# Kernel tuning notes

Measured on AMD Instinct MI355X. Metric: run time of the kernel, lower is better.

## Reference

```python
import jax, jax.numpy as jnp
import numpy as np

N = 5000      # nodes
E = 80000     # edges (avg degree 16)
B = 8         # batch of graph signals sharing one graph
IN = 30       # input feature dim (10 steps x 3)
H = 4         # attention heads
D = 64        # hidden dim per head
HD = H * D    # 256
OUT = 3       # output features per step
NUM_GAT_LAYERS = 4  # num_layer=5 -> 1 + (5-2) layers
EPS = 1e-5


def setup_inputs() -> dict:
    key = jax.random.key(0)
    ks = jax.random.split(key, 40)
    inp = {}
    inp["xx"] = jax.random.normal(ks[0], (B, N, IN), dtype=jnp.float32)
    inp["src"] = jax.random.randint(ks[1], (E,), 0, N, dtype=jnp.int32)
    inp["dst"] = jax.random.randint(ks[2], (E,), 0, N, dtype=jnp.int32)
    dims = [IN, HD, HD, HD]
    k = 3
    for l in range(NUM_GAT_LAYERS):
        fan_in = dims[l]
        inp[f"W{l}"] = jax.random.normal(ks[k], (fan_in, HD), dtype=jnp.float32) / np.sqrt(fan_in); k += 1
        inp[f"al{l}"] = jax.random.normal(ks[k], (H, D), dtype=jnp.float32) * 0.1; k += 1
        inp[f"ar{l}"] = jax.random.normal(ks[k], (H, D), dtype=jnp.float32) * 0.1; k += 1
        inp[f"gamma{l}"] = jnp.ones((HD,), dtype=jnp.float32)
        inp[f"beta{l}"] = jnp.zeros((HD,), dtype=jnp.float32)
    inp["W_out"] = jax.random.normal(ks[k], (HD, OUT), dtype=jnp.float32) / np.sqrt(HD); k += 1
    inp["b_out"] = jnp.zeros((OUT,), dtype=jnp.float32)
    inp["output_length"] = 5
    return inp


def _gat_conv(x, W, al, ar, src, dst):
    # DGL GATConv: fc -> per-head attn logits -> edge softmax over dst -> scatter-sum
    h = (x @ W).reshape(N, H, D)                       # [N,H,D]
    el = (h * al).sum(-1)                              # [N,H]
    er = (h * ar).sum(-1)                              # [N,H]
    e = jax.nn.leaky_relu(el[src] + er[dst], 0.2)      # [E,H]
    m = jax.ops.segment_max(e, dst, num_segments=N)    # [N,H] (stable softmax)
    ex = jnp.exp(e - m[dst])                           # [E,H]
    s = jax.ops.segment_sum(ex, dst, num_segments=N)   # [N,H]
    alpha = ex / s[dst]                                # [E,H]
    return jax.ops.segment_sum(alpha[:, :, None] * h[src], dst, num_segments=N)  # [N,H,D]


def _gat_layer(x, W, al, ar, gamma, beta, src, dst):
    # per-sample GATConv, flatten heads, BatchNorm1d (training stats) over (B,N), LeakyReLU
    out = jax.vmap(lambda xb: _gat_conv(xb, W, al, ar, src, dst))(x)  # [B,N,H,D]
    out = out.reshape(B, N, HD)
    mu = out.mean(axis=(0, 1))
    var = out.var(axis=(0, 1))  # biased, matches torch BN normalization
    out = (out - mu) * jax.lax.rsqrt(var + EPS) * gamma + beta
    return jax.nn.leaky_relu(out, 0.01)


def reference(xx, src, dst,
              W0, al0, ar0, gamma0, beta0,
              W1, al1, ar1, gamma1, beta1,
              W2, al2, ar2, gamma2, beta2,
              W3, al3, ar3, gamma3, beta3,
              W_out, b_out, output_length):
    layers = [(W0, al0, ar0, gamma0, beta0),
              (W1, al1, ar1, gamma1, beta1),
              (W2, al2, ar2, gamma2, beta2),
              (W3, al3, ar3, gamma3, beta3)]
    outputs = []
    for _ in range(output_length):
        h = xx
        for (W, al, ar, g, b) in layers:
            h = _gat_layer(h, W, al, ar, g, b, src, dst)
        out = h @ W_out + b_out                      # [B,N,OUT]
        xx = jnp.concatenate([xx[:, :, 3:], out], axis=-1)
        outputs.append(out[:, :, None, :])
    return jnp.concatenate(outputs, axis=2)          # [B,N,T,OUT]
```

## Files before the change

### kernel.cpp

```cpp
#include <hip/hip_runtime.h>
#include <math.h>

#define NNODES 5000
#define NEDGES 80000
#define NB 8
#define NIN 30
#define K0PAD 32
#define NH 4
#define ND 64
#define NHD 256
#define NT 5
#define NOUT 3
#define ROWS (NB * NNODES)
#define BNEPS 1e-5f
#define KP 40
#define NREP 64
#define BM 32
#define CSTR 264

#define GLOBAL_AS __attribute__((address_space(1)))
#define LDS_AS __attribute__((address_space(3)))

typedef short shortx8 __attribute__((ext_vector_type(8)));
typedef _Float16 halfx8 __attribute__((ext_vector_type(8)));
typedef _Float16 halfx4 __attribute__((ext_vector_type(4)));
typedef _Float16 halfx2 __attribute__((ext_vector_type(2)));
typedef float floatx4 __attribute__((ext_vector_type(4)));
typedef int intx4 __attribute__((ext_vector_type(4)));

static __device__ __forceinline__ unsigned short f2h(float f) {
    union { _Float16 h; unsigned short u; } v;
    v.h = (_Float16)f;
    return v.u;
}
static __device__ __forceinline__ float h2f(unsigned short u) {
    union { _Float16 h; unsigned short u; } v;
    v.u = u;
    return (float)v.h;
}
static __device__ __forceinline__ halfx8 splat8(_Float16 x) {
    return (halfx8){x, x, x, x, x, x, x, x};
}


__global__ void count_kernel(const int* __restrict__ dst, int* __restrict__ counts, int n) {
    int e = blockIdx.x * blockDim.x + threadIdx.x;
    if (e < n) atomicAdd(&counts[dst[e]], 1);
}

__global__ __launch_bounds__(1024) void scan_kernel(const int* __restrict__ counts,
                                                    int* __restrict__ offsets, int n) {
    __shared__ int smem[1024];
    const int CH = 5;
    int tid = threadIdx.x;
    int base = tid * CH;
    int loc[CH];
    int s = 0;
    for (int j = 0; j < CH; ++j) {
        int i = base + j;
        int v = (i < n) ? counts[i] : 0;
        loc[j] = s;
        s += v;
    }
    smem[tid] = s;
    __syncthreads();
    for (int off = 1; off < 1024; off <<= 1) {
        int v = (tid >= off) ? smem[tid - off] : 0;
        __syncthreads();
        smem[tid] += v;
        __syncthreads();
    }
    int excl = smem[tid] - s;
    for (int j = 0; j < CH; ++j) {
        int i = base + j;
        if (i < n) offsets[i] = excl + loc[j];
    }
    if (tid == 1023) offsets[n] = smem[1023];
}

__global__ void fill_kernel(const int* __restrict__ src, const int* __restrict__ dst,
                            const int* __restrict__ offsets, int* __restrict__ cursor,
                            int* __restrict__ csr_src, int n) {
    int e = blockIdx.x * blockDim.x + threadIdx.x;
    if (e >= n) return;
    int d = dst[e];
    int pos = offsets[d] + atomicAdd(&cursor[d], 1);
    csr_src[pos] = src[e];
}


__global__ void pack_all_kernel(const float* __restrict__ xx,
                                const float* __restrict__ W0, const float* __restrict__ W1,
                                const float* __restrict__ W2, const float* __restrict__ W3,
                                unsigned short* __restrict__ xx16,
                                unsigned short* __restrict__ P0, unsigned short* __restrict__ P1,
                                unsigned short* __restrict__ P2, unsigned short* __restrict__ P3) {
    int l = blockIdx.y;
    if (l == 4) {
        for (int idx = blockIdx.x * 256 + threadIdx.x; idx < ROWS * K0PAD; idx += 256 * 256) {
            int g = idx >> 5;
            int k = idx & 31;
            float v = (k < NIN) ? xx[(size_t)g * NIN + k] : 0.0f;
            xx16[idx] = f2h(v);
        }
        return;
    }
    const float* W = (l == 0) ? W0 : (l == 1) ? W1 : (l == 2) ? W2 : W3;
    unsigned short* WtP = (l == 0) ? P0 : (l == 1) ? P1 : (l == 2) ? P2 : P3;
    int Kin = (l == 0) ? NIN : NHD;
    int Kpad = (l == 0) ? K0PAD : NHD;
    int n = blockIdx.x;
    int k = threadIdx.x;
    if (k < Kpad) {
        float v = (k < Kin) ? W[(size_t)k * NHD + n] : 0.0f;
        int t = k >> 5;
        int quad = (k >> 3) & 3;
        int j = k & 7;
        int p = n * 4 + (quad ^ ((n >> 1) & 3));
        WtP[(size_t)t * (NHD * 32) + p * 8 + j] = f2h(v);
    }
}


__global__ __launch_bounds__(256) void bnfinal_kernel(float* __restrict__ sums,
                                                      const float* __restrict__ gamma,
                                                      const float* __restrict__ beta,
                                                      float* __restrict__ bnss) {
    int c = threadIdx.x;
    float s = 0.0f, s2 = 0.0f;
#pragma unroll
    for (int r = 0; r < NREP; ++r) {
        s += sums[r * 2 * NHD + c];
        s2 += sums[r * 2 * NHD + NHD + c];
        sums[r * 2 * NHD + c] = 0.0f;
        sums[r * 2 * NHD + NHD + c] = 0.0f;
    }
    const float invn = 1.0f / (float)ROWS;
    float mu = s * invn;
    float var = s2 * invn - mu * mu;
    float sc = rsqrtf(var + BNEPS) * gamma[c];
    bnss[c] = sc;
    bnss[NHD + c] = beta[c] - mu * sc;
}


__global__ __launch_bounds__(256) void gemm_mfma_kernel(
    const unsigned short* __restrict__ A, const unsigned short* __restrict__ Wt,
    const float* __restrict__ alw, const float* __restrict__ arw,
    const float* __restrict__ bnss, int apply_bn,
    unsigned short* __restrict__ C16, float* __restrict__ el, float* __restrict__ er,
    int K) {
    __shared__ __align__(16) short smem_s[BM * KP + NHD * 32];
    __shared__ __align__(16) unsigned short bnsc16[NHD];
    __shared__ __align__(16) unsigned short bnsh16[NHD];
    short* As = smem_s;
    short* Bs = smem_s + BM * KP;
    int tid = threadIdx.x;
    if (apply_bn) {
        bnsc16[tid] = f2h(bnss[tid]);
        bnsh16[tid] = f2h(bnss[NHD + tid]);
    }
    __syncthreads();

    int wave = tid >> 6;
    int lane = tid & 63;
    int c = lane & 15;
    int quad = lane >> 4;
    int xorv = (c >> 1) & 3;
    int row0 = blockIdx.x * BM;

    floatx4 acc[2][4];
#pragma unroll
    for (int mt = 0; mt < 2; ++mt)
#pragma unroll
        for (int nt = 0; nt < 4; ++nt) acc[mt][nt] = (floatx4){0.f, 0.f, 0.f, 0.f};

    int r = tid >> 2;
    int seg = tid & 3;
    const halfx8 p01 = splat8((_Float16)0.01f);
    for (int k0 = 0; k0 < K; k0 += 32) {
        const unsigned short* gB = Wt + (size_t)(k0 >> 5) * (NHD * 32);
#pragma unroll
        for (int i = 0; i < 4; ++i) {
            int ci = i * 256 + tid;
            __builtin_amdgcn_global_load_lds(
                (const GLOBAL_AS unsigned int*)(gB + ci * 8),
                (LDS_AS unsigned int*)(&Bs[ci * 8]), 16, 0, 0);
        }
        if (r < BM) {
            shortx8 v = *(const shortx8*)(A + (size_t)(row0 + r) * K + k0 + seg * 8);
            if (apply_bn) {
                halfx8 hv = *(halfx8*)&v;
                int kg = k0 + seg * 8;
                halfx8 sc = *(const halfx8*)(&bnsc16[kg]);
                halfx8 sh = *(const halfx8*)(&bnsh16[kg]);
                halfx8 x = hv * sc + sh;
                hv = __builtin_elementwise_max(x, x * p01);
                v = *(shortx8*)&hv;
            }
            *(shortx8*)(&As[r * KP + seg * 8]) = v;
        }
        __syncthreads();
        halfx8 a[2], b[4];
#pragma unroll
        for (int mt = 0; mt < 2; ++mt)
            a[mt] = *(const halfx8*)(&As[(mt * 16 + c) * KP + quad * 8]);
#pragma unroll
        for (int nt = 0; nt < 4; ++nt) {
            int pq = (wave * 64 + nt * 16 + c) * 4 + (quad ^ xorv);
            b[nt] = *(const halfx8*)(&Bs[pq * 8]);
        }
#pragma unroll
        for (int mt = 0; mt < 2; ++mt)
#pragma unroll
            for (int nt = 0; nt < 4; ++nt)
                acc[mt][nt] = __builtin_amdgcn_mfma_f32_16x16x32_f16(a[mt], b[nt],
                                                                     acc[mt][nt], 0, 0, 0);
        __syncthreads();
    }

    short* Cs = smem_s;
    float alv[4], arv[4];
#pragma unroll
    for (int nt = 0; nt < 4; ++nt) {
        alv[nt] = alw[wave * 64 + nt * 16 + c];
        arv[nt] = arw[wave * 64 + nt * 16 + c];
    }
#pragma unroll
    for (int mt = 0; mt < 2; ++mt) {
#pragma unroll
        for (int rr = 0; rr < 4; ++rr) {
            int rl = mt * 16 + quad * 4 + rr;
            int row = row0 + rl;
            float pl = 0.0f, pr = 0.0f;
#pragma unroll
            for (int nt = 0; nt < 4; ++nt) {
                float v = acc[mt][nt][rr];
                Cs[rl * CSTR + wave * 64 + nt * 16 + c] = (short)f2h(v);
                pl += v * alv[nt];
                pr += v * arv[nt];
            }
#pragma unroll
            for (int o = 1; o < 16; o <<= 1) {
                pl += __shfl_xor(pl, o);
                pr += __shfl_xor(pr, o);
            }
            if (c == mt * 4 + rr) {
                el[(size_t)row * NH + wave] = pl;
                er[(size_t)row * NH + wave] = pr;
            }
        }
    }
    __syncthreads();
#pragma unroll
    for (int i = 0; i < 4; ++i) {
        int rl = i * 8 + (tid >> 5);
        int col = (tid & 31) * 8;
        shortx8 vv = *(const shortx8*)(&Cs[rl * CSTR + col]);
        *(shortx8*)(&C16[(size_t)(row0 + rl) * NHD + col]) = vv;
    }
}


__global__ __launch_bounds__(256) void attn_kernel(const unsigned short* __restrict__ h16,
                                                   const float* __restrict__ el,
                                                   const float* __restrict__ er,
                                                   const int* __restrict__ offsets,
                                                   const int* __restrict__ csr_src,
                                                   unsigned short* __restrict__ out16,
                                                   float* __restrict__ sums_cur) {
    __shared__ float bnpart[4][2][NHD];
    int p = blockIdx.x;
    int tid = threadIdx.x;
    int b = p & 7;
    int wave = tid >> 6;
    int lane = tid & 63;
    int head = lane >> 4;
    int li = lane & 15;
    int n = ((p >> 3) << 2) + wave;
    int g = b * NNODES + n;
    int start = offsets[n];
    int deg = offsets[n + 1] - start;
    const float* elb = el + (size_t)b * NNODES * NH;
    float er_nh = er[(size_t)g * NH + head];
    float* bw = &bnpart[wave][0][0];

    if (deg == 0) {
        *(unsigned long long*)(out16 + (size_t)g * NHD + lane * 4) = 0ULL;
        int c4 = lane * 4;
#pragma unroll
        for (int j = 0; j < 4; ++j) {
            bw[c4 + j] = 0.0f;
            bw[NHD + c4 + j] = 0.0f;
        }
    } else if (deg <= 64) {
        float e[4], w[4];
        int s[4];
#pragma unroll
        for (int k = 0; k < 4; ++k) {
            int idx = k * 16 + li;
            if (idx < deg) {
                s[k] = csr_src[start + idx];
                float t = elb[s[k] * NH + head] + er_nh;
                e[k] = (t > 0.0f) ? t : 0.2f * t;
            } else {
                s[k] = 0;
                e[k] = -INFINITY;
            }
        }
        float mx = fmaxf(fmaxf(e[0], e[1]), fmaxf(e[2], e[3]));
#pragma unroll
        for (int o = 8; o; o >>= 1) mx = fmaxf(mx, __shfl_xor(mx, o));
        float sm = 0.0f;
#pragma unroll
        for (int k = 0; k < 4; ++k) {
            w[k] = __expf(e[k] - mx);
            sm += w[k];
        }
#pragma unroll
        for (int o = 8; o; o >>= 1) sm += __shfl_xor(sm, o);
        float invsm = 1.0f / sm;
#pragma unroll
        for (int k = 0; k < 4; ++k) w[k] *= invsm;

        int sub = lane >> 5;
        int i32 = lane & 31;
        int hsel = (lane & 24) << 1;
        const unsigned short* hrow = h16 + (size_t)b * NNODES * NHD + i32 * 8;
        halfx8 acc = splat8((_Float16)0.0f);
#define GATHER_CHUNK(K)                                                          \
        if (deg > (K) * 16) {                                                    \
            int cnt = deg - (K) * 16;                                            \
            cnt = (cnt > 16) ? 16 : cnt;                                         \
            int j = 0;                                                           \
            for (; j + 4 <= cnt; j += 4) {                                       \
                int sa = __shfl(s[K], j + sub);                                  \
                float wa = __shfl(w[K], hsel + j + sub);                         \
                int sb = __shfl(s[K], j + 2 + sub);                              \
                float wb = __shfl(w[K], hsel + j + 2 + sub);                     \
                halfx8 ha = *(const halfx8*)(hrow + (size_t)sa * NHD);           \
                halfx8 hb = *(const halfx8*)(hrow + (size_t)sb * NHD);           \
                acc += ha * splat8((_Float16)wa);                                \
                acc += hb * splat8((_Float16)wb);                                \
            }                                                                    \
            for (; j < cnt; j += 2) {                                            \
                int e2 = j + sub;                                                \
                bool valid = (e2 < cnt);                                         \
                int ec = valid ? e2 : (cnt - 1);                                 \
                int sa = __shfl(s[K], ec);                                       \
                float wa0 = __shfl(w[K], hsel + ec);                             \
                float wa = valid ? wa0 : 0.0f;                                   \
                halfx8 ha = *(const halfx8*)(hrow + (size_t)sa * NHD);           \
                acc += ha * splat8((_Float16)wa);                                \
            }                                                                    \
        }
        GATHER_CHUNK(0)
        GATHER_CHUNK(1)
        GATHER_CHUNK(2)
        GATHER_CHUNK(3)
#undef GATHER_CHUNK
        intx4 ai = *(intx4*)&acc;
        intx4 bi;
        bi[0] = __shfl_xor(ai[0], 32);
        bi[1] = __shfl_xor(ai[1], 32);
        bi[2] = __shfl_xor(ai[2], 32);
        bi[3] = __shfl_xor(ai[3], 32);
        acc += *(halfx8*)&bi;
        if (sub == 0) {
            *(halfx8*)(out16 + (size_t)g * NHD + i32 * 8) = acc;
            int c8 = i32 * 8;
#pragma unroll
            for (int j = 0; j < 8; ++j) {
                float v = (float)acc[j];
                bw[c8 + j] = v;
                bw[NHD + c8 + j] = v * v;
            }
        }
    } else {
        const unsigned short* hbase = h16 + (size_t)b * NNODES * NHD + lane * 4;
        float mx = -INFINITY;
        for (int i = li; i < deg; i += 16) {
            int s2 = csr_src[start + i];
            float t = elb[s2 * NH + head] + er_nh;
            t = (t > 0.0f) ? t : 0.2f * t;
            mx = fmaxf(mx, t);
        }
#pragma unroll
        for (int o = 8; o; o >>= 1) mx = fmaxf(mx, __shfl_xor(mx, o));
        float sm = 0.0f;
        for (int i = li; i < deg; i += 16) {
            int s2 = csr_src[start + i];
            float t = elb[s2 * NH + head] + er_nh;
            t = (t > 0.0f) ? t : 0.2f * t;
            sm += __expf(t - mx);
        }
#pragma unroll
        for (int o = 8; o; o >>= 1) sm += __shfl_xor(sm, o);
        float a0 = 0.f, a1 = 0.f, a2 = 0.f, a3 = 0.f;
        for (int j = 0; j < deg; ++j) {
            int s2 = csr_src[start + j];
            float t = elb[s2 * NH + head] + er_nh;
            t = (t > 0.0f) ? t : 0.2f * t;
            float wj = __expf(t - mx);
            halfx4 hv = *(const halfx4*)(hbase + (size_t)s2 * NHD);
            a0 += wj * (float)hv[0];
            a1 += wj * (float)hv[1];
            a2 += wj * (float)hv[2];
            a3 += wj * (float)hv[3];
        }
        float inv = 1.0f / sm;
        halfx4 o4;
        o4[0] = (_Float16)(a0 * inv);
        o4[1] = (_Float16)(a1 * inv);
        o4[2] = (_Float16)(a2 * inv);
        o4[3] = (_Float16)(a3 * inv);
        *(halfx4*)(out16 + (size_t)g * NHD + lane * 4) = o4;
        int c4 = lane * 4;
#pragma unroll
        for (int j = 0; j < 4; ++j) {
            float v = (float)o4[j];
            bw[c4 + j] = v;
            bw[NHD + c4 + j] = v * v;
        }
    }
    __syncthreads();
    {
        int c = tid;
        float s = bnpart[0][0][c] + bnpart[1][0][c] + bnpart[2][0][c] + bnpart[3][0][c];
        float s2 = bnpart[0][1][c] + bnpart[1][1][c] + bnpart[2][1][c] + bnpart[3][1][c];
        float* sr = sums_cur + (p & (NREP - 1)) * 2 * NHD;
        atomicAdd(&sr[c], s);
        atomicAdd(&sr[NHD + c], s2);
    }
}


__global__ __launch_bounds__(256) void headout_kernel(const unsigned short* __restrict__ x16,
                                                      const float* __restrict__ bnss,
                                                      const float* __restrict__ Wout,
                                                      const float* __restrict__ bout,
                                                      float* __restrict__ out,
                                                      unsigned short* __restrict__ xx16, int t) {
    __shared__ float bsc[NHD];
    __shared__ float bsh[NHD];
    {
        int c = threadIdx.x;
        bsc[c] = bnss[c];
        bsh[c] = bnss[NHD + c];
    }
    __syncthreads();

    int wave = threadIdx.x >> 6;
    int lane = threadIdx.x & 63;
    int g = blockIdx.x * 4 + wave;
    int c0 = lane * 4;
    halfx4 hv = *(const halfx4*)(x16 + (size_t)g * NHD + c0);
    float vv[4];
#pragma unroll
    for (int j = 0; j < 4; ++j) {
        float x = fmaf((float)hv[j], bsc[c0 + j], bsh[c0 + j]);
        vv[j] = (x > 0.0f) ? x : 0.01f * x;
    }
    float r0 = vv[0] * Wout[(c0 + 0) * NOUT + 0] + vv[1] * Wout[(c0 + 1) * NOUT + 0] +
               vv[2] * Wout[(c0 + 2) * NOUT + 0] + vv[3] * Wout[(c0 + 3) * NOUT + 0];
    float r1 = vv[0] * Wout[(c0 + 0) * NOUT + 1] + vv[1] * Wout[(c0 + 1) * NOUT + 1] +
               vv[2] * Wout[(c0 + 2) * NOUT + 1] + vv[3] * Wout[(c0 + 3) * NOUT + 1];
    float r2 = vv[0] * Wout[(c0 + 0) * NOUT + 2] + vv[1] * Wout[(c0 + 1) * NOUT + 2] +
               vv[2] * Wout[(c0 + 2) * NOUT + 2] + vv[3] * Wout[(c0 + 3) * NOUT + 2];
#pragma unroll
    for (int o = 32; o; o >>= 1) {
        r0 += __shfl_xor(r0, o);
        r1 += __shfl_xor(r1, o);
        r2 += __shfl_xor(r2, o);
    }
    float o0 = r0 + bout[0], o1 = r1 + bout[1], o2 = r2 + bout[2];
    if (lane == 0) {
        float* op = out + ((size_t)g * NT + t) * NOUT;
        op[0] = o0;
        op[1] = o1;
        op[2] = o2;
    }
    float oldv = (lane < NIN) ? h2f(xx16[(size_t)g * K0PAD + lane]) : 0.0f;
    float shifted = __shfl(oldv, lane + 3);
    float newv = (lane < 27) ? shifted : (lane == 27 ? o0 : (lane == 28 ? o1 : o2));
    if (lane < NIN) xx16[(size_t)g * K0PAD + lane] = f2h(newv);
}


extern "C" void kernel_launch(void* const* d_in, const int* in_sizes, int n_in,
                              void* d_out, int out_size, void* d_ws, size_t ws_size,
                              hipStream_t stream) {
    const float* xx = (const float*)d_in[0];
    const int* src = (const int*)d_in[1];
    const int* dst = (const int*)d_in[2];
    const float* W[4] = {(const float*)d_in[3], (const float*)d_in[8],
                         (const float*)d_in[13], (const float*)d_in[18]};
    const float* al[4] = {(const float*)d_in[4], (const float*)d_in[9],
                          (const float*)d_in[14], (const float*)d_in[19]};
    const float* ar[4] = {(const float*)d_in[5], (const float*)d_in[10],
                          (const float*)d_in[15], (const float*)d_in[20]};
    const float* gamma[4] = {(const float*)d_in[6], (const float*)d_in[11],
                             (const float*)d_in[16], (const float*)d_in[21]};
    const float* beta[4] = {(const float*)d_in[7], (const float*)d_in[12],
                            (const float*)d_in[17], (const float*)d_in[22]};
    const float* W_out = (const float*)d_in[23];
    const float* b_out = (const float*)d_in[24];
    float* out = (float*)d_out;

    float* wsf = (float*)d_ws;
    float* el = wsf;
    float* er = el + (size_t)ROWS * NH;
    float* sums = er + (size_t)ROWS * NH;
    float* bnss = sums + NREP * 2 * NHD;
    unsigned short* h16 = (unsigned short*)(bnss + 2 * NHD);
    unsigned short* act16 = h16 + (size_t)ROWS * NHD;
    unsigned short* xx16 = act16 + (size_t)ROWS * NHD;
    unsigned short* Wt0 = xx16 + (size_t)ROWS * K0PAD;
    unsigned short* Wt1 = Wt0 + 256 * K0PAD;
    unsigned short* Wt2 = Wt1 + 256 * NHD;
    unsigned short* Wt3 = Wt2 + 256 * NHD;
    int* counts = (int*)(Wt3 + 256 * NHD);
    int* offsets = counts + NNODES;
    int* cursor = offsets + NNODES + 8;
    int* csr_src = cursor + NNODES;
    const unsigned short* Wt[4] = {Wt0, Wt1, Wt2, Wt3};

    hipMemsetAsync(counts, 0, NNODES * sizeof(int), stream);
    hipMemsetAsync(sums, 0, NREP * 2 * NHD * sizeof(float), stream);
    count_kernel<<<(NEDGES + 255) / 256, 256, 0, stream>>>(dst, counts, NEDGES);
    scan_kernel<<<1, 1024, 0, stream>>>(counts, offsets, NNODES);
    hipMemsetAsync(cursor, 0, NNODES * sizeof(int), stream);
    fill_kernel<<<(NEDGES + 255) / 256, 256, 0, stream>>>(src, dst, offsets, cursor,
                                                          csr_src, NEDGES);
    pack_all_kernel<<<dim3(256, 5), 256, 0, stream>>>(xx, W[0], W[1], W[2], W[3],
                                                      xx16,
                                                      (unsigned short*)Wt0,
                                                      (unsigned short*)Wt1,
                                                      (unsigned short*)Wt2,
                                                      (unsigned short*)Wt3);

    for (int t = 0; t < NT; ++t) {
        for (int l = 0; l < 4; ++l) {
            const unsigned short* A16 = (l == 0) ? xx16 : act16;
            int K = (l == 0) ? K0PAD : NHD;
            int apply_bn = (l > 0) ? 1 : 0;
            gemm_mfma_kernel<<<ROWS / BM, 256, 0, stream>>>(A16, Wt[l], al[l], ar[l],
                                                            bnss, apply_bn,
                                                            h16, el, er, K);
            attn_kernel<<<ROWS / 4, 256, 0, stream>>>(h16, el, er, offsets, csr_src,
                                                      act16, sums);
            bnfinal_kernel<<<1, 256, 0, stream>>>(sums, gamma[l], beta[l], bnss);
        }
        headout_kernel<<<ROWS / 4, 256, 0, stream>>>(act16, bnss, W_out, b_out,
                                                     out, xx16, t);
    }
}
```

Before: 1.323 ms.

## Widen attention blocks to eight nodes, swizzle BN partials, fold memsets into pack

The attention kernel now processes eight destination nodes per 512-thread block instead of four. This halves the number of per-block BN-statistic atomic flushes, and the final reduction is split so each thread sums one channel of either the mean or the square. The LDS writes of per-wave BN partials use an XOR swizzle to reduce bank conflicts. Separately, the three setup memsets are folded into an extra slice of the pack kernel, and bnfinal runs as two 128-thread blocks. The larger blocks may lower occupancy, and the node-to-block mapping assumes NNODES is divisible by eight, which holds for 5000.

```diff
diff --git a/kernel.cpp b/kernel.cpp
--- a/kernel.cpp
+++ b/kernel.cpp
@@ -18,6 +18,8 @@
 #define BM 32
 #define CSTR 264
 
+#define BPOS(c) (((c) & ~7) | (((c) & 7) ^ (((c) >> 5) & 7)))
+
 #define GLOBAL_AS __attribute__((address_space(1)))
 #define LDS_AS __attribute__((address_space(3)))
 
@@ -94,7 +96,9 @@
                                 const float* __restrict__ W2, const float* __restrict__ W3,
                                 unsigned short* __restrict__ xx16,
                                 unsigned short* __restrict__ P0, unsigned short* __restrict__ P1,
-                                unsigned short* __restrict__ P2, unsigned short* __restrict__ P3) {
+                                unsigned short* __restrict__ P2, unsigned short* __restrict__ P3,
+                                int* __restrict__ counts, int* __restrict__ cursor,
+                                float* __restrict__ sums) {
     int l = blockIdx.y;
     if (l == 4) {
         for (int idx = blockIdx.x * 256 + threadIdx.x; idx < ROWS * K0PAD; idx += 256 * 256) {
@@ -103,6 +107,15 @@
             float v = (k < NIN) ? xx[(size_t)g * NIN + k] : 0.0f;
             xx16[idx] = f2h(v);
         }
+        return;
+    }
+    if (l == 5) {
+        int ti = blockIdx.x * 256 + threadIdx.x;
+        for (int i = ti; i < 2 * NNODES; i += 256 * 256) {
+            if (i < NNODES) counts[i] = 0;
+            else cursor[i - NNODES] = 0;
+        }
+        for (int i = ti; i < NREP * 2 * NHD; i += 256 * 256) sums[i] = 0.0f;
         return;
     }
     const float* W = (l == 0) ? W0 : (l == 1) ? W1 : (l == 2) ? W2 : W3;
@@ -122,13 +135,13 @@
 }
 
 
-__global__ __launch_bounds__(256) void bnfinal_kernel(float* __restrict__ sums,
+__global__ __launch_bounds__(128) void bnfinal_kernel(float* __restrict__ sums,
                                                       const float* __restrict__ gamma,
                                                       const float* __restrict__ beta,
                                                       float* __restrict__ bnss) {
-    int c = threadIdx.x;
+    int c = blockIdx.x * 128 + threadIdx.x;
     float s = 0.0f, s2 = 0.0f;
-#pragma unroll
+#pragma unroll 8
     for (int r = 0; r < NREP; ++r) {
         s += sums[r * 2 * NHD + c];
         s2 += sums[r * 2 * NHD + NHD + c];
@@ -262,14 +275,14 @@
 }
 
 
-__global__ __launch_bounds__(256) void attn_kernel(const unsigned short* __restrict__ h16,
+__global__ __launch_bounds__(512) void attn_kernel(const unsigned short* __restrict__ h16,
                                                    const float* __restrict__ el,
                                                    const float* __restrict__ er,
                                                    const int* __restrict__ offsets,
                                                    const int* __restrict__ csr_src,
                                                    unsigned short* __restrict__ out16,
                                                    float* __restrict__ sums_cur) {
-    __shared__ float bnpart[4][2][NHD];
+    __shared__ float bnpart[8][2][NHD];
     int p = blockIdx.x;
     int tid = threadIdx.x;
     int b = p & 7;
@@ -277,7 +290,7 @@
     int lane = tid & 63;
     int head = lane >> 4;
     int li = lane & 15;
-    int n = ((p >> 3) << 2) + wave;
+    int n = ((p >> 3) << 3) + wave;
     int g = b * NNODES + n;
     int start = offsets[n];
     int deg = offsets[n + 1] - start;
@@ -290,8 +303,8 @@
         int c4 = lane * 4;
 #pragma unroll
         for (int j = 0; j < 4; ++j) {
-            bw[c4 + j] = 0.0f;
-            bw[NHD + c4 + j] = 0.0f;
+            bw[BPOS(c4 + j)] = 0.0f;
+            bw[NHD + BPOS(c4 + j)] = 0.0f;
         }
     } else if (deg <= 64) {
         float e[4], w[4];
@@ -334,10 +347,10 @@
             cnt = (cnt > 16) ? 16 : cnt;                                         \
             int j = 0;                                                           \
             for (; j + 4 <= cnt; j += 4) {                                       \
-                int sa = __shfl(s[K], j + sub);                                  \
-                float wa = __shfl(w[K], hsel + j + sub);                         \
-                int sb = __shfl(s[K], j + 2 + sub);                              \
-                float wb = __shfl(w[K], hsel + j + 2 + sub);                     \
+                int sa = __shfl(s[K], j + sub, 64);                              \
+                float wa = __shfl(w[K], hsel + j + sub, 64);                     \
+                int sb = __shfl(s[K], j + 2 + sub, 64);                          \
+                float wb = __shfl(w[K], hsel + j + 2 + sub, 64);                 \
                 halfx8 ha = *(const halfx8*)(hrow + (size_t)sa * NHD);           \
                 halfx8 hb = *(const halfx8*)(hrow + (size_t)sb * NHD);           \
                 acc += ha * splat8((_Float16)wa);                                \
@@ -347,8 +360,8 @@
                 int e2 = j + sub;                                                \
                 bool valid = (e2 < cnt);                                         \
                 int ec = valid ? e2 : (cnt - 1);                                 \
-                int sa = __shfl(s[K], ec);                                       \
-                float wa0 = __shfl(w[K], hsel + ec);                             \
+                int sa = __shfl(s[K], ec, 64);                                   \
+                float wa0 = __shfl(w[K], hsel + ec, 64);                         \
                 float wa = valid ? wa0 : 0.0f;                                   \
                 halfx8 ha = *(const halfx8*)(hrow + (size_t)sa * NHD);           \
                 acc += ha * splat8((_Float16)wa);                                \
@@ -361,19 +374,20 @@
 #undef GATHER_CHUNK
         intx4 ai = *(intx4*)&acc;
         intx4 bi;
-        bi[0] = __shfl_xor(ai[0], 32);
-        bi[1] = __shfl_xor(ai[1], 32);
-        bi[2] = __shfl_xor(ai[2], 32);
-        bi[3] = __shfl_xor(ai[3], 32);
+        bi[0] = __shfl_xor(ai[0], 32, 64);
+        bi[1] = __shfl_xor(ai[1], 32, 64);
+        bi[2] = __shfl_xor(ai[2], 32, 64);
+        bi[3] = __shfl_xor(ai[3], 32, 64);
         acc += *(halfx8*)&bi;
         if (sub == 0) {
             *(halfx8*)(out16 + (size_t)g * NHD + i32 * 8) = acc;
             int c8 = i32 * 8;
+            int xj = (i32 >> 2) & 7;
 #pragma unroll
             for (int j = 0; j < 8; ++j) {
                 float v = (float)acc[j];
-                bw[c8 + j] = v;
-                bw[NHD + c8 + j] = v * v;
+                bw[c8 + (j ^ xj)] = v;
+                bw[NHD + c8 + (j ^ xj)] = v * v;
             }
         }
     } else {
@@ -419,18 +433,20 @@
 #pragma unroll
         for (int j = 0; j < 4; ++j) {
             float v = (float)o4[j];
-            bw[c4 + j] = v;
-            bw[NHD + c4 + j] = v * v;
+            bw[BPOS(c4 + j)] = v;
+            bw[NHD + BPOS(c4 + j)] = v * v;
         }
     }
     __syncthreads();
     {
-        int c = tid;
-        float s = bnpart[0][0][c] + bnpart[1][0][c] + bnpart[2][0][c] + bnpart[3][0][c];
-        float s2 = bnpart[0][1][c] + bnpart[1][1][c] + bnpart[2][1][c] + bnpart[3][1][c];
+        int c = tid & 255;
+        int half = tid >> 8;
+        int pc = BPOS(c);
+        float s = 0.0f;
+#pragma unroll
+        for (int w2 = 0; w2 < 8; ++w2) s += bnpart[w2][half][pc];
         float* sr = sums_cur + (p & (NREP - 1)) * 2 * NHD;
-        atomicAdd(&sr[c], s);
-        atomicAdd(&sr[NHD + c], s2);
+        atomicAdd(&sr[half * NHD + c], s);
     }
 }
 
@@ -525,19 +541,17 @@
     int* csr_src = cursor + NNODES;
     const unsigned short* Wt[4] = {Wt0, Wt1, Wt2, Wt3};
 
-    hipMemsetAsync(counts, 0, NNODES * sizeof(int), stream);
-    hipMemsetAsync(sums, 0, NREP * 2 * NHD * sizeof(float), stream);
-    count_kernel<<<(NEDGES + 255) / 256, 256, 0, stream>>>(dst, counts, NEDGES);
-    scan_kernel<<<1, 1024, 0, stream>>>(counts, offsets, NNODES);
-    hipMemsetAsync(cursor, 0, NNODES * sizeof(int), stream);
-    fill_kernel<<<(NEDGES + 255) / 256, 256, 0, stream>>>(src, dst, offsets, cursor,
-                                                          csr_src, NEDGES);
-    pack_all_kernel<<<dim3(256, 5), 256, 0, stream>>>(xx, W[0], W[1], W[2], W[3],
+    pack_all_kernel<<<dim3(256, 6), 256, 0, stream>>>(xx, W[0], W[1], W[2], W[3],
                                                       xx16,
                                                       (unsigned short*)Wt0,
                                                       (unsigned short*)Wt1,
                                                       (unsigned short*)Wt2,
-                                                      (unsigned short*)Wt3);
+                                                      (unsigned short*)Wt3,
+                                                      counts, cursor, sums);
+    count_kernel<<<(NEDGES + 255) / 256, 256, 0, stream>>>(dst, counts, NEDGES);
+    scan_kernel<<<1, 1024, 0, stream>>>(counts, offsets, NNODES);
+    fill_kernel<<<(NEDGES + 255) / 256, 256, 0, stream>>>(src, dst, offsets, cursor,
+                                                          csr_src, NEDGES);
 
     for (int t = 0; t < NT; ++t) {
         for (int l = 0; l < 4; ++l) {
@@ -547,9 +561,9 @@
             gemm_mfma_kernel<<<ROWS / BM, 256, 0, stream>>>(A16, Wt[l], al[l], ar[l],
                                                             bnss, apply_bn,
                                                             h16, el, er, K);
-            attn_kernel<<<ROWS / 4, 256, 0, stream>>>(h16, el, er, offsets, csr_src,
+            attn_kernel<<<ROWS / 8, 512, 0, stream>>>(h16, el, er, offsets, csr_src,
                                                       act16, sums);
-            bnfinal_kernel<<<1, 256, 0, stream>>>(sums, gamma[l], beta[l], bnss);
+            bnfinal_kernel<<<2, 128, 0, stream>>>(sums, gamma[l], beta[l], bnss);
         }
         headout_kernel<<<ROWS / 4, 256, 0, stream>>>(act16, bnss, W_out, b_out,
                                                      out, xx16, t);
```

New measurement: 1.277 ms, median of 2. 1.04x faster.
